# Kernel optimization log

Hardware: AMD Instinct MI355X
Metric: run time of the kernel (lower is better)

## Reference

```python
import jax, jax.numpy as jnp
import numpy as np

F_OUT = 256      # out_channels
NH = 8           # num_heads
DH = F_OUT // NH # head dim = 32
KH = KW = 8      # kernel (window) size == stride == q_stride
KK = KH * KW     # 64 keys per window


def setup_inputs() -> dict:
    key = jax.random.key(0)
    k1, k2, k3 = jax.random.split(key, 3)
    x = jax.random.normal(k1, (8, 256, 128, 128), jnp.float32)
    # 1x1 conv weight for qkv projection, xavier-ish scale
    proj_w = jax.random.normal(k2, (3 * F_OUT, 256), jnp.float32) * (1.0 / np.sqrt(256.0))
    proj_b = jnp.zeros((3 * F_OUT,), jnp.float32)
    # learned position features (module inits to zeros; use small random for a nontrivial test)
    pos_feats = jax.random.normal(k3, (F_OUT, KK), jnp.float32) * 0.02
    return {"x": x, "proj_w": proj_w, "proj_b": proj_b, "pos_feats": pos_feats}


def reference(x, proj_w, proj_b, pos_feats):
    B, C, H, W = x.shape
    f = F_OUT
    # 1x1 conv == channel GEMM: [B,3f,H,W]
    qkv = jnp.einsum('bchw,oc->bohw', x, proj_w) + proj_b[None, :, None, None]
    scale = float(f // NH) ** (-0.25)
    # query: slice every q_stride-th position -> [B,f,Hq,Wq]
    q = qkv[:, :f, ::KH, ::KW]
    kv = qkv[:, f:3 * f]                       # [B,2f,H,W]
    Hq, Wq = H // KH, W // KW
    # non-overlapping window unfold (stride==kernel, padding=0, dilation=1)
    # -> [B,Hq,Wq,2f,KK], matching torch as_strided(...).reshape(..., -1)
    kv = kv.reshape(B, 2 * f, Hq, KH, Wq, KW)
    kv = kv.transpose(0, 2, 4, 1, 3, 5).reshape(B, Hq, Wq, 2 * f, KK)
    # keys: pos_feats + scale*key, then split heads -> [B,Hq,Wq,NH,DH,KK]
    key_m = (pos_feats + scale * kv[..., :f, :]).reshape(B, Hq, Wq, NH, DH, KK)
    val_m = kv[..., f:2 * f, :].reshape(B, Hq, Wq, NH, DH, KK)
    # queries: scale, channels-last, split heads -> [B,Hq,Wq,NH,DH]
    q_m = (scale * q).transpose(0, 2, 3, 1).reshape(B, Hq, Wq, NH, DH)
    logits = jnp.einsum('bhwnd,bhwndk->bhwnk', q_m, key_m)   # [B,Hq,Wq,NH,KK]
    attn = jax.nn.softmax(logits, axis=-1)
    out = jnp.einsum('bhwnk,bhwndk->bhwnd', attn, val_m)     # [B,Hq,Wq,NH,DH]
    return out.reshape(B, Hq, Wq, f).transpose(0, 3, 1, 2)   # [B,f,Hq,Wq]
```

## Files before the change

kernel.cpp:

```cpp
#include <hip/hip_runtime.h>
#include <hip/hip_bf16.h>
#include <cstdint>
#include <cstddef>

#define SCALE 0.42044820762685725f

typedef __attribute__((ext_vector_type(8))) short short8;
typedef __attribute__((ext_vector_type(4))) short short4v;
typedef __attribute__((ext_vector_type(4))) float f32x4;

__device__ __forceinline__ unsigned int pk2bf(float lo, float hi) {
    __hip_bfloat162 h = __float22bfloat162_rn(float2{lo, hi});
    unsigned int u;
    __builtin_memcpy(&u, &h, sizeof(u));
    return u;
}
__device__ __forceinline__ unsigned short f2bf(float f) {
    unsigned int u = __builtin_bit_cast(unsigned int, f);
    u = (u + 0x7fffu + ((u >> 16) & 1u)) >> 16;
    return (unsigned short)u;
}
__device__ __forceinline__ float bf2f(unsigned short h) {
    unsigned int u = ((unsigned int)h) << 16;
    return __builtin_bit_cast(float, u);
}


__global__ __launch_bounds__(256) void prepack_w(const float* __restrict__ w,
                                                 const float* __restrict__ pos,
                                                 unsigned short* __restrict__ wp,
                                                 unsigned short* __restrict__ pT,
                                                 float* __restrict__ wqT) {
    int gid = blockIdx.x * 256 + threadIdx.x;
    if (gid < 24576) {
        int lane = gid & 63;
        int ks   = (gid >> 6) & 7;
        int mtg  = gid >> 9;
        int row  = (mtg < 32 ? 256 + mtg * 16 : (mtg - 32) * 16) + (lane & 15);
        int k0   = ks * 32 + (lane >> 4) * 8;
        const float* src = w + row * 256 + k0;
        short8 v;
#pragma unroll
        for (int j = 0; j < 8; ++j) v[j] = (short)f2bf(src[j]);
        *reinterpret_cast<short8*>(wp + (size_t)gid * 8) = v;
    } else if (gid < 40960) {
        int u = gid - 24576;
        pT[u] = f2bf(pos[(u & 255) * 64 + (u >> 8)]);
    } else {
        int u = gid - 40960;
        wqT[u] = w[(u & 255) * 256 + (u >> 8)];
    }
}

__global__ __launch_bounds__(256) void q_kernel(const float* __restrict__ x,
                                                const float* __restrict__ wqT,
                                                const float* __restrict__ proj_b,
                                                float* __restrict__ q_all) {
    __shared__ float s_x0[4][256];
    const int t = threadIdx.x;
    const int tile0 = blockIdx.x * 4;
    const int b = tile0 >> 8, hq = (tile0 >> 4) & 15, wq0 = tile0 & 15;
    {
        const float* src = x + (size_t)b * 4194304 + (size_t)t * 16384 + hq * 1024 + wq0 * 8;
#pragma unroll
        for (int j = 0; j < 4; ++j) s_x0[j][t] = src[j * 8];
    }
    __syncthreads();
    float acc[4] = {0.f, 0.f, 0.f, 0.f};
#pragma unroll 8
    for (int c = 0; c < 256; ++c) {
        float wv = wqT[c * 256 + t];
#pragma unroll
        for (int j = 0; j < 4; ++j) acc[j] = fmaf(wv, s_x0[j][c], acc[j]);
    }
    float bq = proj_b[t];
#pragma unroll
    for (int j = 0; j < 4; ++j)
        q_all[(size_t)(tile0 + j) * 256 + t] = SCALE * (acc[j] + bq);
}

template <bool PRE>
__global__ __launch_bounds__(512, 4) void attn_fused(
        const float* __restrict__ x, const float* __restrict__ proj_w,
        const float* __restrict__ proj_b, const float* __restrict__ pos,
        const unsigned short* __restrict__ wpack, const unsigned short* __restrict__ posT,
        const float* __restrict__ q_all, float* __restrict__ out) {
    __shared__ __align__(16) unsigned char s_main[32768];
    __shared__ __align__(16) float s_vbias[256];
    __shared__ __align__(16) float s_qs[256];

    const int t    = threadIdx.x;
    const int lane = t & 63;
    const int wave = t >> 6;
    const int l15  = lane & 15;
    const int l4   = lane >> 4;

    int bid  = blockIdx.x;
    int tile = (bid & 7) * 256 + (bid >> 3);
    int b  = tile >> 8;
    int hq = (tile >> 4) & 15;
    int wq = tile & 15;

    const float* xb = x + (size_t)b * 4194304 + (size_t)(hq * 8) * 128 + wq * 8;

    if (t < 256) s_vbias[t] = proj_b[512 + t];

    {
        const int p   = lane;
        const int pl  = lane & 1;
        const int px0 = lane & ~1;
        const float* xpx = xb + (px0 >> 3) * 128 + (px0 & 7);
        float2 v[16];
#pragma unroll
        for (int g = 0; g < 4; ++g)
#pragma unroll
            for (int j = 0; j < 4; ++j) {
                int c = (g * 8 + wave) * 8 + 2 * j + pl;
                v[g * 4 + j] = *reinterpret_cast<const float2*>(xpx + (size_t)c * 16384);
            }
#pragma unroll
        for (int g = 0; g < 4; ++g) {
            uint4 pk;
            unsigned int* pku = &pk.x;
#pragma unroll
            for (int j = 0; j < 4; ++j) {
                float2 w2 = v[g * 4 + j];
                float sel   = pl ? w2.x : w2.y;
                float other = __shfl_xor(sel, 1);
                pku[j] = pl ? pk2bf(other, w2.y) : pk2bf(w2.x, other);
            }
            int c8 = g * 8 + wave;
            *reinterpret_cast<uint4*>(s_main + p * 512 + ((c8 * 16) ^ ((p & 7) << 4))) = pk;
        }
    }
    __syncthreads();

    f32x4 acc[4][4];
#pragma unroll
    for (int mt = 0; mt < 4; ++mt)
#pragma unroll
        for (int nt = 0; nt < 4; ++nt) acc[mt][nt] = (f32x4){0.f, 0.f, 0.f, 0.f};
    f32x4 accQ[2];
    if (!PRE) {
#pragma unroll
        for (int mt = 0; mt < 2; ++mt) accQ[mt] = (f32x4){0.f, 0.f, 0.f, 0.f};
    }

#pragma unroll 2
    for (int ks = 0; ks < 8; ++ks) {
        short8 bfr[4];
#pragma unroll
        for (int nt = 0; nt < 4; ++nt) {
            int n  = nt * 16 + l15;
            int kb = ks * 32 + l4 * 8;
            bfr[nt] = *reinterpret_cast<const short8*>(
                s_main + n * 512 + ((2 * kb) ^ ((n & 7) << 4)));
        }
        short8 afk[2], afv[2];
#pragma unroll
        for (int mt = 0; mt < 2; ++mt) {
            if (PRE) {
                afk[mt] = *reinterpret_cast<const short8*>(
                    wpack + ((size_t)(((wave * 2 + mt) * 8 + ks) * 64 + lane)) * 8);
                afv[mt] = *reinterpret_cast<const short8*>(
                    wpack + ((size_t)(((16 + wave * 2 + mt) * 8 + ks) * 64 + lane)) * 8);
            } else {
                const float* wk = proj_w + (256 + (wave * 2 + mt) * 16 + l15) * 256 + ks * 32 + l4 * 8;
                const float* wv = proj_w + (512 + (wave * 2 + mt) * 16 + l15) * 256 + ks * 32 + l4 * 8;
#pragma unroll
                for (int j = 0; j < 8; ++j) { afk[mt][j] = (short)f2bf(wk[j]); afv[mt][j] = (short)f2bf(wv[j]); }
            }
        }
#pragma unroll
        for (int mt = 0; mt < 2; ++mt)
#pragma unroll
            for (int nt = 0; nt < 4; ++nt) {
                acc[mt][nt]     = __builtin_amdgcn_mfma_f32_16x16x32_bf16(afk[mt], bfr[nt], acc[mt][nt], 0, 0, 0);
                acc[2 + mt][nt] = __builtin_amdgcn_mfma_f32_16x16x32_bf16(afv[mt], bfr[nt], acc[2 + mt][nt], 0, 0, 0);
            }
        if (!PRE) {
            short8 afq[2];
#pragma unroll
            for (int mt = 0; mt < 2; ++mt) {
                const float* wq2 = proj_w + ((wave * 2 + mt) * 16 + l15) * 256 + ks * 32 + l4 * 8;
#pragma unroll
                for (int j = 0; j < 8; ++j) afq[mt][j] = (short)f2bf(wq2[j]);
                accQ[mt] = __builtin_amdgcn_mfma_f32_16x16x32_bf16(afq[mt], bfr[0], accQ[mt], 0, 0, 0);
            }
        }
    }

    if (!PRE) {
        if (l15 == 0) {
#pragma unroll
            for (int mt = 0; mt < 2; ++mt)
#pragma unroll
                for (int i = 0; i < 4; ++i) {
                    int row = wave * 32 + mt * 16 + l4 * 4 + i;
                    s_qs[row] = SCALE * (accQ[mt][i] + proj_b[row]);
                }
        }
    }

    float attnw[4];
    {
        float qf[2][4];
        if (PRE) {
            const float* qp = q_all + (size_t)tile * 256 + wave * 32 + l4 * 4;
#pragma unroll
            for (int mt = 0; mt < 2; ++mt) {
                float4 qv = *reinterpret_cast<const float4*>(qp + mt * 16);
                qf[mt][0] = qv.x; qf[mt][1] = qv.y; qf[mt][2] = qv.z; qf[mt][3] = qv.w;
            }
        } else {
#pragma unroll
            for (int mt = 0; mt < 2; ++mt)
#pragma unroll
                for (int i = 0; i < 4; ++i) qf[mt][i] = s_qs[wave * 32 + mt * 16 + l4 * 4 + i];
        }
        short4v pos4[4][2];
        if (PRE) {
#pragma unroll
            for (int nt = 0; nt < 4; ++nt)
#pragma unroll
                for (int mt = 0; mt < 2; ++mt)
                    pos4[nt][mt] = *reinterpret_cast<const short4v*>(
                        posT + (size_t)(nt * 16 + l15) * 256 + wave * 32 + mt * 16 + l4 * 4);
        }

        float lg[4];
#pragma unroll
        for (int nt = 0; nt < 4; ++nt) {
            float p = 0.f;
#pragma unroll
            for (int mt = 0; mt < 2; ++mt)
#pragma unroll
                for (int i = 0; i < 4; ++i) {
                    float pf = PRE ? bf2f((unsigned short)pos4[nt][mt][i])
                                   : pos[(size_t)(wave * 32 + mt * 16 + l4 * 4 + i) * 64 + nt * 16 + l15];
                    p = fmaf(qf[mt][i], fmaf(SCALE, acc[mt][nt][i], pf), p);
                }
            p += __shfl_xor(p, 16);
            p += __shfl_xor(p, 32);
            lg[nt] = p;
        }
        float mx = fmaxf(fmaxf(lg[0], lg[1]), fmaxf(lg[2], lg[3]));
        mx = fmaxf(mx, __shfl_xor(mx, 1));
        mx = fmaxf(mx, __shfl_xor(mx, 2));
        mx = fmaxf(mx, __shfl_xor(mx, 4));
        mx = fmaxf(mx, __shfl_xor(mx, 8));
        float e0 = __expf(lg[0] - mx), e1 = __expf(lg[1] - mx);
        float e2 = __expf(lg[2] - mx), e3 = __expf(lg[3] - mx);
        float s = (e0 + e1) + (e2 + e3);
        s += __shfl_xor(s, 1);
        s += __shfl_xor(s, 2);
        s += __shfl_xor(s, 4);
        s += __shfl_xor(s, 8);
        float rs = 1.f / s;
        attnw[0] = e0 * rs; attnw[1] = e1 * rs; attnw[2] = e2 * rs; attnw[3] = e3 * rs;
    }

#pragma unroll
    for (int mt = 0; mt < 2; ++mt) {
#pragma unroll
        for (int i = 0; i < 4; ++i) {
            float sum = attnw[0] * acc[2 + mt][0][i] + attnw[1] * acc[2 + mt][1][i]
                      + attnw[2] * acc[2 + mt][2][i] + attnw[3] * acc[2 + mt][3][i];
            sum += __shfl_xor(sum, 1);
            sum += __shfl_xor(sum, 2);
            sum += __shfl_xor(sum, 4);
            sum += __shfl_xor(sum, 8);
            if (l15 == 0) {
                int vr = wave * 32 + mt * 16 + l4 * 4 + i;
                out[(size_t)b * 65536 + (size_t)vr * 256 + hq * 16 + wq] = sum + s_vbias[vr];
            }
        }
    }
}

extern "C" void kernel_launch(void* const* d_in, const int* in_sizes, int n_in,
                              void* d_out, int out_size, void* d_ws, size_t ws_size,
                              hipStream_t stream) {
    (void)in_sizes; (void)n_in; (void)out_size;
    const float* x      = (const float*)d_in[0];
    const float* proj_w = (const float*)d_in[1];
    const float* proj_b = (const float*)d_in[2];
    const float* pos    = (const float*)d_in[3];
    float* out = (float*)d_out;

    const size_t OFF_POST = 393216;
    const size_t OFF_WQT  = 425984;
    const size_t OFF_QALL = 688128;
    const size_t need_ws  = OFF_QALL + 2097152;

    if (d_ws != nullptr && ws_size >= need_ws) {
        unsigned short* wp  = (unsigned short*)d_ws;
        unsigned short* pT  = (unsigned short*)((char*)d_ws + OFF_POST);
        float*          wqT = (float*)((char*)d_ws + OFF_WQT);
        float*          qA  = (float*)((char*)d_ws + OFF_QALL);
        prepack_w<<<416, 256, 0, stream>>>(proj_w, pos, wp, pT, wqT);
        q_kernel<<<512, 256, 0, stream>>>(x, wqT, proj_b, qA);
        attn_fused<true><<<2048, 512, 0, stream>>>(x, proj_w, proj_b, pos, wp, pT, qA, out);
    } else {
        attn_fused<false><<<2048, 512, 0, stream>>>(x, proj_w, proj_b, pos, nullptr, nullptr, nullptr, out);
    }
}
```

Measured before the change: 85.44 us.

## Make attention kernel persistent over 8 tiles with register-resident weights and double-buffered x

Each block now processes 8 consecutive windows instead of one, launching 256 blocks instead of 2048. The K/V weight fragments are loaded into registers once per block rather than reloaded every k-step for every window. The next window's x slab is prefetched into registers during the softmax/output phase and written to a second LDS buffer, overlapping global loads with compute. This raises register pressure (launch bounds lowered to 2 blocks per CU), and 256 blocks of 8 waves may underfill the GPU's CUs.

```diff
diff --git a/kernel.cpp b/kernel.cpp
--- a/kernel.cpp
+++ b/kernel.cpp
@@ -80,12 +80,12 @@
 }
 
 template <bool PRE>
-__global__ __launch_bounds__(512, 4) void attn_fused(
+__global__ __launch_bounds__(512, 2) void attn_fused(
         const float* __restrict__ x, const float* __restrict__ proj_w,
         const float* __restrict__ proj_b, const float* __restrict__ pos,
         const unsigned short* __restrict__ wpack, const unsigned short* __restrict__ posT,
         const float* __restrict__ q_all, float* __restrict__ out) {
-    __shared__ __align__(16) unsigned char s_main[32768];
+    __shared__ __align__(16) unsigned char s_x[2][32768];
     __shared__ __align__(16) float s_vbias[256];
     __shared__ __align__(16) float s_qs[256];
 
@@ -95,22 +95,46 @@
     const int l15  = lane & 15;
     const int l4   = lane >> 4;
 
-    int bid  = blockIdx.x;
-    int tile = (bid & 7) * 256 + (bid >> 3);
-    int b  = tile >> 8;
-    int hq = (tile >> 4) & 15;
-    int wq = tile & 15;
-
-    const float* xb = x + (size_t)b * 4194304 + (size_t)(hq * 8) * 128 + wq * 8;
+    const int bid   = blockIdx.x;
+    const int tile0 = (bid & 7) * 256 + (bid >> 3) * 8;
+    const int b   = tile0 >> 8;
+    const int hq  = (tile0 >> 4) & 15;
+    const int wq0 = tile0 & 15;
 
     if (t < 256) s_vbias[t] = proj_b[512 + t];
 
-    {
-        const int p   = lane;
-        const int pl  = lane & 1;
-        const int px0 = lane & ~1;
-        const float* xpx = xb + (px0 >> 3) * 128 + (px0 & 7);
-        float2 v[16];
+    short8 wK[2][8], wV[2][8];
+    if (PRE) {
+#pragma unroll
+        for (int mt = 0; mt < 2; ++mt)
+#pragma unroll
+            for (int ks = 0; ks < 8; ++ks) {
+                wK[mt][ks] = *reinterpret_cast<const short8*>(
+                    wpack + ((size_t)(((wave * 2 + mt) * 8 + ks) * 64 + lane)) * 8);
+                wV[mt][ks] = *reinterpret_cast<const short8*>(
+                    wpack + ((size_t)(((16 + wave * 2 + mt) * 8 + ks) * 64 + lane)) * 8);
+            }
+    } else {
+#pragma unroll
+        for (int mt = 0; mt < 2; ++mt)
+#pragma unroll
+            for (int ks = 0; ks < 8; ++ks) {
+                const float* wk = proj_w + (256 + (wave * 2 + mt) * 16 + l15) * 256 + ks * 32 + l4 * 8;
+                const float* wv = proj_w + (512 + (wave * 2 + mt) * 16 + l15) * 256 + ks * 32 + l4 * 8;
+#pragma unroll
+                for (int j = 0; j < 8; ++j) {
+                    wK[mt][ks][j] = (short)f2bf(wk[j]);
+                    wV[mt][ks][j] = (short)f2bf(wv[j]);
+                }
+            }
+    }
+
+    const int pl  = lane & 1;
+    const int px0 = lane & ~1;
+    auto issue_x = [&](int tile, float2* v) {
+        const int wq = tile & 15;
+        const float* xpx = x + (size_t)b * 4194304 + (size_t)(hq * 8) * 128 + wq * 8
+                             + (px0 >> 3) * 128 + (px0 & 7);
 #pragma unroll
         for (int g = 0; g < 4; ++g)
 #pragma unroll
@@ -118,6 +142,10 @@
                 int c = (g * 8 + wave) * 8 + 2 * j + pl;
                 v[g * 4 + j] = *reinterpret_cast<const float2*>(xpx + (size_t)c * 16384);
             }
+    };
+    auto write_x = [&](int buf, const float2* v) {
+        const int p = lane;
+        unsigned char* base = s_x[buf];
 #pragma unroll
         for (int g = 0; g < 4; ++g) {
             uint4 pk;
@@ -130,81 +158,77 @@
                 pku[j] = pl ? pk2bf(other, w2.y) : pk2bf(w2.x, other);
             }
             int c8 = g * 8 + wave;
-            *reinterpret_cast<uint4*>(s_main + p * 512 + ((c8 * 16) ^ ((p & 7) << 4))) = pk;
-        }
+            *reinterpret_cast<uint4*>(base + p * 512 + ((c8 * 16) ^ ((p & 7) << 4))) = pk;
+        }
+    };
+
+    {
+        float2 v0[16];
+        issue_x(tile0, v0);
+        write_x(0, v0);
     }
     __syncthreads();
 
-    f32x4 acc[4][4];
-#pragma unroll
-    for (int mt = 0; mt < 4; ++mt)
-#pragma unroll
-        for (int nt = 0; nt < 4; ++nt) acc[mt][nt] = (f32x4){0.f, 0.f, 0.f, 0.f};
-    f32x4 accQ[2];
-    if (!PRE) {
-#pragma unroll
-        for (int mt = 0; mt < 2; ++mt) accQ[mt] = (f32x4){0.f, 0.f, 0.f, 0.f};
-    }
-
-#pragma unroll 2
-    for (int ks = 0; ks < 8; ++ks) {
-        short8 bfr[4];
-#pragma unroll
-        for (int nt = 0; nt < 4; ++nt) {
-            int n  = nt * 16 + l15;
-            int kb = ks * 32 + l4 * 8;
-            bfr[nt] = *reinterpret_cast<const short8*>(
-                s_main + n * 512 + ((2 * kb) ^ ((n & 7) << 4)));
-        }
-        short8 afk[2], afv[2];
-#pragma unroll
-        for (int mt = 0; mt < 2; ++mt) {
-            if (PRE) {
-                afk[mt] = *reinterpret_cast<const short8*>(
-                    wpack + ((size_t)(((wave * 2 + mt) * 8 + ks) * 64 + lane)) * 8);
-                afv[mt] = *reinterpret_cast<const short8*>(
-                    wpack + ((size_t)(((16 + wave * 2 + mt) * 8 + ks) * 64 + lane)) * 8);
-            } else {
-                const float* wk = proj_w + (256 + (wave * 2 + mt) * 16 + l15) * 256 + ks * 32 + l4 * 8;
-                const float* wv = proj_w + (512 + (wave * 2 + mt) * 16 + l15) * 256 + ks * 32 + l4 * 8;
-#pragma unroll
-                for (int j = 0; j < 8; ++j) { afk[mt][j] = (short)f2bf(wk[j]); afv[mt][j] = (short)f2bf(wv[j]); }
-            }
-        }
-#pragma unroll
-        for (int mt = 0; mt < 2; ++mt)
+#pragma unroll 1
+    for (int ti = 0; ti < 8; ++ti) {
+        const int tile = tile0 + ti;
+        const int wq   = wq0 + ti;
+        const unsigned char* xl = s_x[ti & 1];
+
+        f32x4 acc[4][4];
+#pragma unroll
+        for (int mt = 0; mt < 4; ++mt)
+#pragma unroll
+            for (int nt = 0; nt < 4; ++nt) acc[mt][nt] = (f32x4){0.f, 0.f, 0.f, 0.f};
+        f32x4 accQ[2];
+        if (!PRE) {
+#pragma unroll
+            for (int mt = 0; mt < 2; ++mt) accQ[mt] = (f32x4){0.f, 0.f, 0.f, 0.f};
+        }
+
+#pragma unroll
+        for (int ks = 0; ks < 8; ++ks) {
+            short8 bfr[4];
 #pragma unroll
             for (int nt = 0; nt < 4; ++nt) {
-                acc[mt][nt]     = __builtin_amdgcn_mfma_f32_16x16x32_bf16(afk[mt], bfr[nt], acc[mt][nt], 0, 0, 0);
-                acc[2 + mt][nt] = __builtin_amdgcn_mfma_f32_16x16x32_bf16(afv[mt], bfr[nt], acc[2 + mt][nt], 0, 0, 0);
-            }
+                int n  = nt * 16 + l15;
+                int kb = ks * 32 + l4 * 8;
+                bfr[nt] = *reinterpret_cast<const short8*>(
+                    xl + n * 512 + ((2 * kb) ^ ((n & 7) << 4)));
+            }
+#pragma unroll
+            for (int mt = 0; mt < 2; ++mt)
+#pragma unroll
+                for (int nt = 0; nt < 4; ++nt) {
+                    acc[mt][nt]     = __builtin_amdgcn_mfma_f32_16x16x32_bf16(wK[mt][ks], bfr[nt], acc[mt][nt], 0, 0, 0);
+                    acc[2 + mt][nt] = __builtin_amdgcn_mfma_f32_16x16x32_bf16(wV[mt][ks], bfr[nt], acc[2 + mt][nt], 0, 0, 0);
+                }
+            if (!PRE) {
+                short8 afq[2];
+#pragma unroll
+                for (int mt = 0; mt < 2; ++mt) {
+                    const float* wq2 = proj_w + ((wave * 2 + mt) * 16 + l15) * 256 + ks * 32 + l4 * 8;
+#pragma unroll
+                    for (int j = 0; j < 8; ++j) afq[mt][j] = (short)f2bf(wq2[j]);
+                    accQ[mt] = __builtin_amdgcn_mfma_f32_16x16x32_bf16(afq[mt], bfr[0], accQ[mt], 0, 0, 0);
+                }
+            }
+        }
+
         if (!PRE) {
-            short8 afq[2];
-#pragma unroll
-            for (int mt = 0; mt < 2; ++mt) {
-                const float* wq2 = proj_w + ((wave * 2 + mt) * 16 + l15) * 256 + ks * 32 + l4 * 8;
-#pragma unroll
-                for (int j = 0; j < 8; ++j) afq[mt][j] = (short)f2bf(wq2[j]);
-                accQ[mt] = __builtin_amdgcn_mfma_f32_16x16x32_bf16(afq[mt], bfr[0], accQ[mt], 0, 0, 0);
-            }
-        }
-    }
-
-    if (!PRE) {
-        if (l15 == 0) {
-#pragma unroll
-            for (int mt = 0; mt < 2; ++mt)
-#pragma unroll
-                for (int i = 0; i < 4; ++i) {
-                    int row = wave * 32 + mt * 16 + l4 * 4 + i;
-                    s_qs[row] = SCALE * (accQ[mt][i] + proj_b[row]);
-                }
-        }
-    }
-
-    float attnw[4];
-    {
+            if (l15 == 0) {
+#pragma unroll
+                for (int mt = 0; mt < 2; ++mt)
+#pragma unroll
+                    for (int i = 0; i < 4; ++i) {
+                        int row = wave * 32 + mt * 16 + l4 * 4 + i;
+                        s_qs[row] = SCALE * (accQ[mt][i] + proj_b[row]);
+                    }
+            }
+        }
+
         float qf[2][4];
+        short4v pos4[4][2];
         if (PRE) {
             const float* qp = q_all + (size_t)tile * 256 + wave * 32 + l4 * 4;
 #pragma unroll
@@ -212,14 +236,6 @@
                 float4 qv = *reinterpret_cast<const float4*>(qp + mt * 16);
                 qf[mt][0] = qv.x; qf[mt][1] = qv.y; qf[mt][2] = qv.z; qf[mt][3] = qv.w;
             }
-        } else {
-#pragma unroll
-            for (int mt = 0; mt < 2; ++mt)
-#pragma unroll
-                for (int i = 0; i < 4; ++i) qf[mt][i] = s_qs[wave * 32 + mt * 16 + l4 * 4 + i];
-        }
-        short4v pos4[4][2];
-        if (PRE) {
 #pragma unroll
             for (int nt = 0; nt < 4; ++nt)
 #pragma unroll
@@ -228,53 +244,69 @@
                         posT + (size_t)(nt * 16 + l15) * 256 + wave * 32 + mt * 16 + l4 * 4);
         }
 
-        float lg[4];
-#pragma unroll
-        for (int nt = 0; nt < 4; ++nt) {
-            float p = 0.f;
+        float2 v[16];
+        if (ti < 7) issue_x(tile + 1, v);
+
+        if (!PRE) {
 #pragma unroll
             for (int mt = 0; mt < 2; ++mt)
 #pragma unroll
-                for (int i = 0; i < 4; ++i) {
-                    float pf = PRE ? bf2f((unsigned short)pos4[nt][mt][i])
-                                   : pos[(size_t)(wave * 32 + mt * 16 + l4 * 4 + i) * 64 + nt * 16 + l15];
-                    p = fmaf(qf[mt][i], fmaf(SCALE, acc[mt][nt][i], pf), p);
+                for (int i = 0; i < 4; ++i) qf[mt][i] = s_qs[wave * 32 + mt * 16 + l4 * 4 + i];
+        }
+
+        float attnw[4];
+        {
+            float lg[4];
+#pragma unroll
+            for (int nt = 0; nt < 4; ++nt) {
+                float p = 0.f;
+#pragma unroll
+                for (int mt = 0; mt < 2; ++mt)
+#pragma unroll
+                    for (int i = 0; i < 4; ++i) {
+                        float pf = PRE ? bf2f((unsigned short)pos4[nt][mt][i])
+                                       : pos[(size_t)(wave * 32 + mt * 16 + l4 * 4 + i) * 64 + nt * 16 + l15];
+                        p = fmaf(qf[mt][i], fmaf(SCALE, acc[mt][nt][i], pf), p);
+                    }
+                p += __shfl_xor(p, 16);
+                p += __shfl_xor(p, 32);
+                lg[nt] = p;
+            }
+            float mx = fmaxf(fmaxf(lg[0], lg[1]), fmaxf(lg[2], lg[3]));
+            mx = fmaxf(mx, __shfl_xor(mx, 1));
+            mx = fmaxf(mx, __shfl_xor(mx, 2));
+            mx = fmaxf(mx, __shfl_xor(mx, 4));
+            mx = fmaxf(mx, __shfl_xor(mx, 8));
+            float e0 = __expf(lg[0] - mx), e1 = __expf(lg[1] - mx);
+            float e2 = __expf(lg[2] - mx), e3 = __expf(lg[3] - mx);
+            float s = (e0 + e1) + (e2 + e3);
+            s += __shfl_xor(s, 1);
+            s += __shfl_xor(s, 2);
+            s += __shfl_xor(s, 4);
+            s += __shfl_xor(s, 8);
+            float rs = 1.f / s;
+            attnw[0] = e0 * rs; attnw[1] = e1 * rs; attnw[2] = e2 * rs; attnw[3] = e3 * rs;
+        }
+
+#pragma unroll
+        for (int mt = 0; mt < 2; ++mt) {
+#pragma unroll
+            for (int i = 0; i < 4; ++i) {
+                float sum = attnw[0] * acc[2 + mt][0][i] + attnw[1] * acc[2 + mt][1][i]
+                          + attnw[2] * acc[2 + mt][2][i] + attnw[3] * acc[2 + mt][3][i];
+                sum += __shfl_xor(sum, 1);
+                sum += __shfl_xor(sum, 2);
+                sum += __shfl_xor(sum, 4);
+                sum += __shfl_xor(sum, 8);
+                if (l15 == 0) {
+                    int vr = wave * 32 + mt * 16 + l4 * 4 + i;
+                    out[(size_t)b * 65536 + (size_t)vr * 256 + hq * 16 + wq] = sum + s_vbias[vr];
                 }
-            p += __shfl_xor(p, 16);
-            p += __shfl_xor(p, 32);
-            lg[nt] = p;
-        }
-        float mx = fmaxf(fmaxf(lg[0], lg[1]), fmaxf(lg[2], lg[3]));
-        mx = fmaxf(mx, __shfl_xor(mx, 1));
-        mx = fmaxf(mx, __shfl_xor(mx, 2));
-        mx = fmaxf(mx, __shfl_xor(mx, 4));
-        mx = fmaxf(mx, __shfl_xor(mx, 8));
-        float e0 = __expf(lg[0] - mx), e1 = __expf(lg[1] - mx);
-        float e2 = __expf(lg[2] - mx), e3 = __expf(lg[3] - mx);
-        float s = (e0 + e1) + (e2 + e3);
-        s += __shfl_xor(s, 1);
-        s += __shfl_xor(s, 2);
-        s += __shfl_xor(s, 4);
-        s += __shfl_xor(s, 8);
-        float rs = 1.f / s;
-        attnw[0] = e0 * rs; attnw[1] = e1 * rs; attnw[2] = e2 * rs; attnw[3] = e3 * rs;
-    }
-
-#pragma unroll
-    for (int mt = 0; mt < 2; ++mt) {
-#pragma unroll
-        for (int i = 0; i < 4; ++i) {
-            float sum = attnw[0] * acc[2 + mt][0][i] + attnw[1] * acc[2 + mt][1][i]
-                      + attnw[2] * acc[2 + mt][2][i] + attnw[3] * acc[2 + mt][3][i];
-            sum += __shfl_xor(sum, 1);
-            sum += __shfl_xor(sum, 2);
-            sum += __shfl_xor(sum, 4);
-            sum += __shfl_xor(sum, 8);
-            if (l15 == 0) {
-                int vr = wave * 32 + mt * 16 + l4 * 4 + i;
-                out[(size_t)b * 65536 + (size_t)vr * 256 + hq * 16 + wq] = sum + s_vbias[vr];
-            }
-        }
+            }
+        }
+
+        if (ti < 7) write_x((ti & 1) ^ 1, v);
+        __syncthreads();
     }
 }
 
@@ -300,8 +332,8 @@
         float*          qA  = (float*)((char*)d_ws + OFF_QALL);
         prepack_w<<<416, 256, 0, stream>>>(proj_w, pos, wp, pT, wqT);
         q_kernel<<<512, 256, 0, stream>>>(x, wqT, proj_b, qA);
-        attn_fused<true><<<2048, 512, 0, stream>>>(x, proj_w, proj_b, pos, wp, pT, qA, out);
+        attn_fused<true><<<256, 512, 0, stream>>>(x, proj_w, proj_b, pos, wp, pT, qA, out);
     } else {
-        attn_fused<false><<<2048, 512, 0, stream>>>(x, proj_w, proj_b, pos, nullptr, nullptr, nullptr, out);
-    }
-}
+        attn_fused<false><<<256, 512, 0, stream>>>(x, proj_w, proj_b, pos, nullptr, nullptr, nullptr, out);
+    }
+}
```

Result: slower. 230.3 us (+169.6%).

## Split heads across two blocks per tile with separate K and V waves

Applied to the files above, without the earlier changes.

Each window tile is now handled by two blocks, each covering four heads. Within a block, waves 0-3 compute keys and softmax while waves 4-7 compute values, and the attention weights pass between them through shared memory. This halves per-wave accumulator registers so occupancy can go up (launch bounds raised to 5). The cost is that every block still loads and converts the full 8x8x256 input window, so x traffic and conversion work double, and an extra barrier is added.

```diff
diff --git a/kernel.cpp b/kernel.cpp
--- a/kernel.cpp
+++ b/kernel.cpp
@@ -80,13 +80,14 @@
 }
 
 template <bool PRE>
-__global__ __launch_bounds__(512, 4) void attn_fused(
+__global__ __launch_bounds__(512, 5) void attn_fused(
         const float* __restrict__ x, const float* __restrict__ proj_w,
         const float* __restrict__ proj_b, const float* __restrict__ pos,
         const unsigned short* __restrict__ wpack, const unsigned short* __restrict__ posT,
         const float* __restrict__ q_all, float* __restrict__ out) {
     __shared__ __align__(16) unsigned char s_main[32768];
     __shared__ __align__(16) float s_vbias[256];
+    __shared__ __align__(16) float s_attn[4][64];
     __shared__ __align__(16) float s_qs[256];
 
     const int t    = threadIdx.x;
@@ -95,13 +96,18 @@
     const int l15  = lane & 15;
     const int l4   = lane >> 4;
 
-    int bid  = blockIdx.x;
-    int tile = (bid & 7) * 256 + (bid >> 3);
-    int b  = tile >> 8;
-    int hq = (tile >> 4) & 15;
-    int wq = tile & 15;
-
-    const float* xb = x + (size_t)b * 4194304 + (size_t)(hq * 8) * 128 + wq * 8;
+    const int bid  = blockIdx.x;
+    const int xcd  = bid & 7;
+    const int idx  = bid >> 3;
+    const int tin  = idx >> 1;
+    const int half = idx & 1;
+    const int b  = xcd;
+    const int hq = tin >> 4;
+    const int wq = tin & 15;
+    const int tile = xcd * 256 + tin;
+
+    const int head = half * 4 + (wave & 3);
+    const bool isK = wave < 4;
 
     if (t < 256) s_vbias[t] = proj_b[512 + t];
 
@@ -109,7 +115,8 @@
         const int p   = lane;
         const int pl  = lane & 1;
         const int px0 = lane & ~1;
-        const float* xpx = xb + (px0 >> 3) * 128 + (px0 & 7);
+        const float* xpx = x + (size_t)b * 4194304 + (size_t)(hq * 8) * 128 + wq * 8
+                             + (px0 >> 3) * 128 + (px0 & 7);
         float2 v[16];
 #pragma unroll
         for (int g = 0; g < 4; ++g)
@@ -135,16 +142,18 @@
     }
     __syncthreads();
 
-    f32x4 acc[4][4];
-#pragma unroll
-    for (int mt = 0; mt < 4; ++mt)
+    f32x4 acc[2][4];
+#pragma unroll
+    for (int mt = 0; mt < 2; ++mt)
 #pragma unroll
         for (int nt = 0; nt < 4; ++nt) acc[mt][nt] = (f32x4){0.f, 0.f, 0.f, 0.f};
     f32x4 accQ[2];
-    if (!PRE) {
+    if (!PRE && isK) {
 #pragma unroll
         for (int mt = 0; mt < 2; ++mt) accQ[mt] = (f32x4){0.f, 0.f, 0.f, 0.f};
     }
+
+    const int mtg0 = (isK ? 0 : 16) + head * 2;
 
 #pragma unroll 2
     for (int ks = 0; ks < 8; ++ks) {
@@ -156,33 +165,29 @@
             bfr[nt] = *reinterpret_cast<const short8*>(
                 s_main + n * 512 + ((2 * kb) ^ ((n & 7) << 4)));
         }
-        short8 afk[2], afv[2];
+        short8 af[2];
 #pragma unroll
         for (int mt = 0; mt < 2; ++mt) {
             if (PRE) {
-                afk[mt] = *reinterpret_cast<const short8*>(
-                    wpack + ((size_t)(((wave * 2 + mt) * 8 + ks) * 64 + lane)) * 8);
-                afv[mt] = *reinterpret_cast<const short8*>(
-                    wpack + ((size_t)(((16 + wave * 2 + mt) * 8 + ks) * 64 + lane)) * 8);
+                af[mt] = *reinterpret_cast<const short8*>(
+                    wpack + ((size_t)(((mtg0 + mt) * 8 + ks) * 64 + lane)) * 8);
             } else {
-                const float* wk = proj_w + (256 + (wave * 2 + mt) * 16 + l15) * 256 + ks * 32 + l4 * 8;
-                const float* wv = proj_w + (512 + (wave * 2 + mt) * 16 + l15) * 256 + ks * 32 + l4 * 8;
-#pragma unroll
-                for (int j = 0; j < 8; ++j) { afk[mt][j] = (short)f2bf(wk[j]); afv[mt][j] = (short)f2bf(wv[j]); }
+                int row = (isK ? 256 : 512) + head * 32 + mt * 16 + l15;
+                const float* src = proj_w + row * 256 + ks * 32 + l4 * 8;
+#pragma unroll
+                for (int j = 0; j < 8; ++j) af[mt][j] = (short)f2bf(src[j]);
             }
         }
 #pragma unroll
         for (int mt = 0; mt < 2; ++mt)
 #pragma unroll
-            for (int nt = 0; nt < 4; ++nt) {
-                acc[mt][nt]     = __builtin_amdgcn_mfma_f32_16x16x32_bf16(afk[mt], bfr[nt], acc[mt][nt], 0, 0, 0);
-                acc[2 + mt][nt] = __builtin_amdgcn_mfma_f32_16x16x32_bf16(afv[mt], bfr[nt], acc[2 + mt][nt], 0, 0, 0);
-            }
-        if (!PRE) {
+            for (int nt = 0; nt < 4; ++nt)
+                acc[mt][nt] = __builtin_amdgcn_mfma_f32_16x16x32_bf16(af[mt], bfr[nt], acc[mt][nt], 0, 0, 0);
+        if (!PRE && isK) {
             short8 afq[2];
 #pragma unroll
             for (int mt = 0; mt < 2; ++mt) {
-                const float* wq2 = proj_w + ((wave * 2 + mt) * 16 + l15) * 256 + ks * 32 + l4 * 8;
+                const float* wq2 = proj_w + (head * 32 + mt * 16 + l15) * 256 + ks * 32 + l4 * 8;
 #pragma unroll
                 for (int j = 0; j < 8; ++j) afq[mt][j] = (short)f2bf(wq2[j]);
                 accQ[mt] = __builtin_amdgcn_mfma_f32_16x16x32_bf16(afq[mt], bfr[0], accQ[mt], 0, 0, 0);
@@ -190,42 +195,38 @@
         }
     }
 
-    if (!PRE) {
-        if (l15 == 0) {
-#pragma unroll
-            for (int mt = 0; mt < 2; ++mt)
-#pragma unroll
-                for (int i = 0; i < 4; ++i) {
-                    int row = wave * 32 + mt * 16 + l4 * 4 + i;
-                    s_qs[row] = SCALE * (accQ[mt][i] + proj_b[row]);
-                }
-        }
-    }
-
-    float attnw[4];
-    {
+    if (isK) {
+        if (!PRE) {
+            if (l15 == 0) {
+#pragma unroll
+                for (int mt = 0; mt < 2; ++mt)
+#pragma unroll
+                    for (int i = 0; i < 4; ++i) {
+                        int row = head * 32 + mt * 16 + l4 * 4 + i;
+                        s_qs[row] = SCALE * (accQ[mt][i] + proj_b[row]);
+                    }
+            }
+        }
         float qf[2][4];
+        short4v pos4[4][2];
         if (PRE) {
-            const float* qp = q_all + (size_t)tile * 256 + wave * 32 + l4 * 4;
+            const float* qp = q_all + (size_t)tile * 256 + head * 32 + l4 * 4;
 #pragma unroll
             for (int mt = 0; mt < 2; ++mt) {
                 float4 qv = *reinterpret_cast<const float4*>(qp + mt * 16);
                 qf[mt][0] = qv.x; qf[mt][1] = qv.y; qf[mt][2] = qv.z; qf[mt][3] = qv.w;
             }
-        } else {
-#pragma unroll
-            for (int mt = 0; mt < 2; ++mt)
-#pragma unroll
-                for (int i = 0; i < 4; ++i) qf[mt][i] = s_qs[wave * 32 + mt * 16 + l4 * 4 + i];
-        }
-        short4v pos4[4][2];
-        if (PRE) {
 #pragma unroll
             for (int nt = 0; nt < 4; ++nt)
 #pragma unroll
                 for (int mt = 0; mt < 2; ++mt)
                     pos4[nt][mt] = *reinterpret_cast<const short4v*>(
-                        posT + (size_t)(nt * 16 + l15) * 256 + wave * 32 + mt * 16 + l4 * 4);
+                        posT + (size_t)(nt * 16 + l15) * 256 + head * 32 + mt * 16 + l4 * 4);
+        } else {
+#pragma unroll
+            for (int mt = 0; mt < 2; ++mt)
+#pragma unroll
+                for (int i = 0; i < 4; ++i) qf[mt][i] = s_qs[head * 32 + mt * 16 + l4 * 4 + i];
         }
 
         float lg[4];
@@ -237,7 +238,7 @@
 #pragma unroll
                 for (int i = 0; i < 4; ++i) {
                     float pf = PRE ? bf2f((unsigned short)pos4[nt][mt][i])
-                                   : pos[(size_t)(wave * 32 + mt * 16 + l4 * 4 + i) * 64 + nt * 16 + l15];
+                                   : pos[(size_t)(head * 32 + mt * 16 + l4 * 4 + i) * 64 + nt * 16 + l15];
                     p = fmaf(qf[mt][i], fmaf(SCALE, acc[mt][nt][i], pf), p);
                 }
             p += __shfl_xor(p, 16);
@@ -257,22 +258,32 @@
         s += __shfl_xor(s, 4);
         s += __shfl_xor(s, 8);
         float rs = 1.f / s;
-        attnw[0] = e0 * rs; attnw[1] = e1 * rs; attnw[2] = e2 * rs; attnw[3] = e3 * rs;
-    }
-
-#pragma unroll
-    for (int mt = 0; mt < 2; ++mt) {
-#pragma unroll
-        for (int i = 0; i < 4; ++i) {
-            float sum = attnw[0] * acc[2 + mt][0][i] + attnw[1] * acc[2 + mt][1][i]
-                      + attnw[2] * acc[2 + mt][2][i] + attnw[3] * acc[2 + mt][3][i];
-            sum += __shfl_xor(sum, 1);
-            sum += __shfl_xor(sum, 2);
-            sum += __shfl_xor(sum, 4);
-            sum += __shfl_xor(sum, 8);
-            if (l15 == 0) {
-                int vr = wave * 32 + mt * 16 + l4 * 4 + i;
-                out[(size_t)b * 65536 + (size_t)vr * 256 + hq * 16 + wq] = sum + s_vbias[vr];
+        if (l4 == 0) {
+            s_attn[head & 3][l15]      = e0 * rs;
+            s_attn[head & 3][16 + l15] = e1 * rs;
+            s_attn[head & 3][32 + l15] = e2 * rs;
+            s_attn[head & 3][48 + l15] = e3 * rs;
+        }
+    }
+    __syncthreads();
+
+    if (!isK) {
+        const float* ap = s_attn[head & 3];
+        float a0 = ap[l15], a1 = ap[16 + l15], a2 = ap[32 + l15], a3 = ap[48 + l15];
+#pragma unroll
+        for (int mt = 0; mt < 2; ++mt) {
+#pragma unroll
+            for (int i = 0; i < 4; ++i) {
+                float sum = a0 * acc[mt][0][i] + a1 * acc[mt][1][i]
+                          + a2 * acc[mt][2][i] + a3 * acc[mt][3][i];
+                sum += __shfl_xor(sum, 1);
+                sum += __shfl_xor(sum, 2);
+                sum += __shfl_xor(sum, 4);
+                sum += __shfl_xor(sum, 8);
+                if (l15 == 0) {
+                    int vr = head * 32 + mt * 16 + l4 * 4 + i;
+                    out[(size_t)b * 65536 + (size_t)vr * 256 + hq * 16 + wq] = sum + s_vbias[vr];
+                }
             }
         }
     }
@@ -300,8 +311,8 @@
         float*          qA  = (float*)((char*)d_ws + OFF_QALL);
         prepack_w<<<416, 256, 0, stream>>>(proj_w, pos, wp, pT, wqT);
         q_kernel<<<512, 256, 0, stream>>>(x, wqT, proj_b, qA);
-        attn_fused<true><<<2048, 512, 0, stream>>>(x, proj_w, proj_b, pos, wp, pT, qA, out);
+        attn_fused<true><<<4096, 512, 0, stream>>>(x, proj_w, proj_b, pos, wp, pT, qA, out);
     } else {
-        attn_fused<false><<<2048, 512, 0, stream>>>(x, proj_w, proj_b, pos, nullptr, nullptr, nullptr, out);
-    }
-}
+        attn_fused<false><<<4096, 512, 0, stream>>>(x, proj_w, proj_b, pos, nullptr, nullptr, nullptr, out);
+    }
+}
```

Result: slower. 97.23 us (+13.8%).

## Process four adjacent windows per block with strip-wide coalesced x loads

Applied to the files above, without the earlier changes.

Each attention block now handles a strip of four horizontally adjacent 8x8 windows. It loads all 32 columns of x rows into four LDS tiles so global reads cover wider contiguous spans, and hoists the pos loads out of the per-tile loop. The q kernel likewise computes 16 query tiles per block, and grid sizes shrink to match. The larger LDS footprint (128KB) and the lower occupancy bound reduce concurrency, and the per-tile work inside a block now runs serially.

```diff
diff --git a/kernel.cpp b/kernel.cpp
--- a/kernel.cpp
+++ b/kernel.cpp
@@ -56,36 +56,38 @@
                                                 const float* __restrict__ wqT,
                                                 const float* __restrict__ proj_b,
                                                 float* __restrict__ q_all) {
-    __shared__ float s_x0[4][256];
+    __shared__ float s_x0[16][256];
     const int t = threadIdx.x;
-    const int tile0 = blockIdx.x * 4;
-    const int b = tile0 >> 8, hq = (tile0 >> 4) & 15, wq0 = tile0 & 15;
+    const int tile0 = blockIdx.x * 16;
+    const int b = tile0 >> 8, hq = (tile0 >> 4) & 15;
     {
-        const float* src = x + (size_t)b * 4194304 + (size_t)t * 16384 + hq * 1024 + wq0 * 8;
-#pragma unroll
-        for (int j = 0; j < 4; ++j) s_x0[j][t] = src[j * 8];
+        const float* src = x + (size_t)b * 4194304 + (size_t)t * 16384 + hq * 1024;
+#pragma unroll
+        for (int j = 0; j < 16; ++j) s_x0[j][t] = src[j * 8];
     }
     __syncthreads();
-    float acc[4] = {0.f, 0.f, 0.f, 0.f};
-#pragma unroll 8
+    float acc[16];
+#pragma unroll
+    for (int j = 0; j < 16; ++j) acc[j] = 0.f;
+#pragma unroll 4
     for (int c = 0; c < 256; ++c) {
         float wv = wqT[c * 256 + t];
 #pragma unroll
-        for (int j = 0; j < 4; ++j) acc[j] = fmaf(wv, s_x0[j][c], acc[j]);
+        for (int j = 0; j < 16; ++j) acc[j] = fmaf(wv, s_x0[j][c], acc[j]);
     }
     float bq = proj_b[t];
 #pragma unroll
-    for (int j = 0; j < 4; ++j)
+    for (int j = 0; j < 16; ++j)
         q_all[(size_t)(tile0 + j) * 256 + t] = SCALE * (acc[j] + bq);
 }
 
 template <bool PRE>
-__global__ __launch_bounds__(512, 4) void attn_fused(
+__global__ __launch_bounds__(512, 2) void attn_fused(
         const float* __restrict__ x, const float* __restrict__ proj_w,
         const float* __restrict__ proj_b, const float* __restrict__ pos,
         const unsigned short* __restrict__ wpack, const unsigned short* __restrict__ posT,
         const float* __restrict__ q_all, float* __restrict__ out) {
-    __shared__ __align__(16) unsigned char s_main[32768];
+    __shared__ __align__(16) unsigned char s_x[4][32768];
     __shared__ __align__(16) float s_vbias[256];
     __shared__ __align__(16) float s_qs[256];
 
@@ -95,184 +97,194 @@
     const int l15  = lane & 15;
     const int l4   = lane >> 4;
 
-    int bid  = blockIdx.x;
-    int tile = (bid & 7) * 256 + (bid >> 3);
-    int b  = tile >> 8;
-    int hq = (tile >> 4) & 15;
-    int wq = tile & 15;
-
-    const float* xb = x + (size_t)b * 4194304 + (size_t)(hq * 8) * 128 + wq * 8;
+    const int bid   = blockIdx.x;
+    const int b     = bid & 7;
+    const int strip = bid >> 3;
+    const int hq    = strip >> 2;
+    const int wq0   = (strip & 3) * 4;
+    const int tile0 = b * 256 + hq * 16 + wq0;
 
     if (t < 256) s_vbias[t] = proj_b[512 + t];
 
+    short4v pos4[4][2];
+    if (PRE) {
+#pragma unroll
+        for (int nt = 0; nt < 4; ++nt)
+#pragma unroll
+            for (int mt = 0; mt < 2; ++mt)
+                pos4[nt][mt] = *reinterpret_cast<const short4v*>(
+                    posT + (size_t)(nt * 16 + l15) * 256 + wave * 32 + mt * 16 + l4 * 4);
+    }
+
     {
-        const int p   = lane;
         const int pl  = lane & 1;
-        const int px0 = lane & ~1;
-        const float* xpx = xb + (px0 >> 3) * 128 + (px0 & 7);
-        float2 v[16];
-#pragma unroll
-        for (int g = 0; g < 4; ++g)
-#pragma unroll
-            for (int j = 0; j < 4; ++j) {
-                int c = (g * 8 + wave) * 8 + 2 * j + pl;
-                v[g * 4 + j] = *reinterpret_cast<const float2*>(xpx + (size_t)c * 16384);
-            }
-#pragma unroll
-        for (int g = 0; g < 4; ++g) {
-            uint4 pk;
-            unsigned int* pku = &pk.x;
-#pragma unroll
-            for (int j = 0; j < 4; ++j) {
-                float2 w2 = v[g * 4 + j];
-                float sel   = pl ? w2.x : w2.y;
+        const int w2  = (lane >> 1) & 15;
+        const int hlo = (lane >> 5) & 1;
+        const int pxs = w2 * 2 + pl;
+        const int til = pxs >> 3;
+        const int px7 = pxs & 7;
+        const float* xs = x + (size_t)b * 4194304 + (size_t)(hq * 8) * 128 + wq0 * 8;
+#pragma unroll 1
+        for (int kb = 0; kb < 8; ++kb) {
+            float2 v[8];
+#pragma unroll
+            for (int u = 0; u < 8; ++u) {
+                int idx = wave * 64 + kb * 8 + u;
+                int c   = (idx & 127) * 2 + pl;
+                int h   = (idx >> 7) * 2 + hlo;
+                v[u] = *reinterpret_cast<const float2*>(xs + (size_t)c * 16384 + h * 128 + w2 * 2);
+            }
+#pragma unroll
+            for (int u = 0; u < 8; ++u) {
+                int idx = wave * 64 + kb * 8 + u;
+                int h   = (idx >> 7) * 2 + hlo;
+                int pin = h * 8 + px7;
+                float sel   = pl ? v[u].x : v[u].y;
                 float other = __shfl_xor(sel, 1);
-                pku[j] = pl ? pk2bf(other, w2.y) : pk2bf(w2.x, other);
-            }
-            int c8 = g * 8 + wave;
-            *reinterpret_cast<uint4*>(s_main + p * 512 + ((c8 * 16) ^ ((p & 7) << 4))) = pk;
+                unsigned int pk = pl ? pk2bf(other, v[u].y) : pk2bf(v[u].x, other);
+                *reinterpret_cast<unsigned int*>(
+                    s_x[til] + pin * 512 + ((4 * (idx & 127)) ^ ((pin & 7) << 4))) = pk;
+            }
         }
     }
     __syncthreads();
 
-    f32x4 acc[4][4];
-#pragma unroll
-    for (int mt = 0; mt < 4; ++mt)
-#pragma unroll
-        for (int nt = 0; nt < 4; ++nt) acc[mt][nt] = (f32x4){0.f, 0.f, 0.f, 0.f};
-    f32x4 accQ[2];
-    if (!PRE) {
-#pragma unroll
-        for (int mt = 0; mt < 2; ++mt) accQ[mt] = (f32x4){0.f, 0.f, 0.f, 0.f};
-    }
+#pragma unroll 1
+    for (int ti = 0; ti < 4; ++ti) {
+        const int tile = tile0 + ti;
+        const int wq   = wq0 + ti;
+        const unsigned char* xl = s_x[ti];
+
+        f32x4 acc[4][4];
+#pragma unroll
+        for (int mt = 0; mt < 4; ++mt)
+#pragma unroll
+            for (int nt = 0; nt < 4; ++nt) acc[mt][nt] = (f32x4){0.f, 0.f, 0.f, 0.f};
+        f32x4 accQ[2];
+        if (!PRE) {
+#pragma unroll
+            for (int mt = 0; mt < 2; ++mt) accQ[mt] = (f32x4){0.f, 0.f, 0.f, 0.f};
+        }
 
 #pragma unroll 2
-    for (int ks = 0; ks < 8; ++ks) {
-        short8 bfr[4];
-#pragma unroll
-        for (int nt = 0; nt < 4; ++nt) {
-            int n  = nt * 16 + l15;
-            int kb = ks * 32 + l4 * 8;
-            bfr[nt] = *reinterpret_cast<const short8*>(
-                s_main + n * 512 + ((2 * kb) ^ ((n & 7) << 4)));
-        }
-        short8 afk[2], afv[2];
+        for (int ks = 0; ks < 8; ++ks) {
+            short8 bfr[4];
+#pragma unroll
+            for (int nt = 0; nt < 4; ++nt) {
+                int n  = nt * 16 + l15;
+                int kb = ks * 32 + l4 * 8;
+                bfr[nt] = *reinterpret_cast<const short8*>(
+                    xl + n * 512 + ((2 * kb) ^ ((n & 7) << 4)));
+            }
+            short8 afk[2], afv[2];
+#pragma unroll
+            for (int mt = 0; mt < 2; ++mt) {
+                if (PRE) {
+                    afk[mt] = *reinterpret_cast<const short8*>(
+                        wpack + ((size_t)(((wave * 2 + mt) * 8 + ks) * 64 + lane)) * 8);
+                    afv[mt] = *reinterpret_cast<const short8*>(
+                        wpack + ((size_t)(((16 + wave * 2 + mt) * 8 + ks) * 64 + lane)) * 8);
+                } else {
+                    const float* wk = proj_w + (256 + (wave * 2 + mt) * 16 + l15) * 256 + ks * 32 + l4 * 8;
+                    const float* wv = proj_w + (512 + (wave * 2 + mt) * 16 + l15) * 256 + ks * 32 + l4 * 8;
+#pragma unroll
+                    for (int j = 0; j < 8; ++j) { afk[mt][j] = (short)f2bf(wk[j]); afv[mt][j] = (short)f2bf(wv[j]); }
+                }
+            }
+#pragma unroll
+            for (int mt = 0; mt < 2; ++mt)
+#pragma unroll
+                for (int nt = 0; nt < 4; ++nt) {
+                    acc[mt][nt]     = __builtin_amdgcn_mfma_f32_16x16x32_bf16(afk[mt], bfr[nt], acc[mt][nt], 0, 0, 0);
+                    acc[2 + mt][nt] = __builtin_amdgcn_mfma_f32_16x16x32_bf16(afv[mt], bfr[nt], acc[2 + mt][nt], 0, 0, 0);
+                }
+            if (!PRE) {
+                short8 afq[2];
+#pragma unroll
+                for (int mt = 0; mt < 2; ++mt) {
+                    const float* wq2 = proj_w + ((wave * 2 + mt) * 16 + l15) * 256 + ks * 32 + l4 * 8;
+#pragma unroll
+                    for (int j = 0; j < 8; ++j) afq[mt][j] = (short)f2bf(wq2[j]);
+                    accQ[mt] = __builtin_amdgcn_mfma_f32_16x16x32_bf16(afq[mt], bfr[0], accQ[mt], 0, 0, 0);
+                }
+            }
+        }
+
+        if (!PRE) {
+            if (l15 == 0) {
+#pragma unroll
+                for (int mt = 0; mt < 2; ++mt)
+#pragma unroll
+                    for (int i = 0; i < 4; ++i) {
+                        int row = wave * 32 + mt * 16 + l4 * 4 + i;
+                        s_qs[row] = SCALE * (accQ[mt][i] + proj_b[row]);
+                    }
+            }
+        }
+
+        float attnw[4];
+        {
+            float qf[2][4];
+            if (PRE) {
+                const float* qp = q_all + (size_t)tile * 256 + wave * 32 + l4 * 4;
+#pragma unroll
+                for (int mt = 0; mt < 2; ++mt) {
+                    float4 qv = *reinterpret_cast<const float4*>(qp + mt * 16);
+                    qf[mt][0] = qv.x; qf[mt][1] = qv.y; qf[mt][2] = qv.z; qf[mt][3] = qv.w;
+                }
+            } else {
+#pragma unroll
+                for (int mt = 0; mt < 2; ++mt)
+#pragma unroll
+                    for (int i = 0; i < 4; ++i) qf[mt][i] = s_qs[wave * 32 + mt * 16 + l4 * 4 + i];
+            }
+
+            float lg[4];
+#pragma unroll
+            for (int nt = 0; nt < 4; ++nt) {
+                float p = 0.f;
+#pragma unroll
+                for (int mt = 0; mt < 2; ++mt)
+#pragma unroll
+                    for (int i = 0; i < 4; ++i) {
+                        float pf = PRE ? bf2f((unsigned short)pos4[nt][mt][i])
+                                       : pos[(size_t)(wave * 32 + mt * 16 + l4 * 4 + i) * 64 + nt * 16 + l15];
+                        p = fmaf(qf[mt][i], fmaf(SCALE, acc[mt][nt][i], pf), p);
+                    }
+                p += __shfl_xor(p, 16);
+                p += __shfl_xor(p, 32);
+                lg[nt] = p;
+            }
+            float mx = fmaxf(fmaxf(lg[0], lg[1]), fmaxf(lg[2], lg[3]));
+            mx = fmaxf(mx, __shfl_xor(mx, 1));
+            mx = fmaxf(mx, __shfl_xor(mx, 2));
+            mx = fmaxf(mx, __shfl_xor(mx, 4));
+            mx = fmaxf(mx, __shfl_xor(mx, 8));
+            float e0 = __expf(lg[0] - mx), e1 = __expf(lg[1] - mx);
+            float e2 = __expf(lg[2] - mx), e3 = __expf(lg[3] - mx);
+            float s = (e0 + e1) + (e2 + e3);
+            s += __shfl_xor(s, 1);
+            s += __shfl_xor(s, 2);
+            s += __shfl_xor(s, 4);
+            s += __shfl_xor(s, 8);
+            float rs = 1.f / s;
+            attnw[0] = e0 * rs; attnw[1] = e1 * rs; attnw[2] = e2 * rs; attnw[3] = e3 * rs;
+        }
+
 #pragma unroll
         for (int mt = 0; mt < 2; ++mt) {
-            if (PRE) {
-                afk[mt] = *reinterpret_cast<const short8*>(
-                    wpack + ((size_t)(((wave * 2 + mt) * 8 + ks) * 64 + lane)) * 8);
-                afv[mt] = *reinterpret_cast<const short8*>(
-                    wpack + ((size_t)(((16 + wave * 2 + mt) * 8 + ks) * 64 + lane)) * 8);
-            } else {
-                const float* wk = proj_w + (256 + (wave * 2 + mt) * 16 + l15) * 256 + ks * 32 + l4 * 8;
-                const float* wv = proj_w + (512 + (wave * 2 + mt) * 16 + l15) * 256 + ks * 32 + l4 * 8;
-#pragma unroll
-                for (int j = 0; j < 8; ++j) { afk[mt][j] = (short)f2bf(wk[j]); afv[mt][j] = (short)f2bf(wv[j]); }
-            }
-        }
-#pragma unroll
-        for (int mt = 0; mt < 2; ++mt)
-#pragma unroll
-            for (int nt = 0; nt < 4; ++nt) {
-                acc[mt][nt]     = __builtin_amdgcn_mfma_f32_16x16x32_bf16(afk[mt], bfr[nt], acc[mt][nt], 0, 0, 0);
-                acc[2 + mt][nt] = __builtin_amdgcn_mfma_f32_16x16x32_bf16(afv[mt], bfr[nt], acc[2 + mt][nt], 0, 0, 0);
-            }
-        if (!PRE) {
-            short8 afq[2];
-#pragma unroll
-            for (int mt = 0; mt < 2; ++mt) {
-                const float* wq2 = proj_w + ((wave * 2 + mt) * 16 + l15) * 256 + ks * 32 + l4 * 8;
-#pragma unroll
-                for (int j = 0; j < 8; ++j) afq[mt][j] = (short)f2bf(wq2[j]);
-                accQ[mt] = __builtin_amdgcn_mfma_f32_16x16x32_bf16(afq[mt], bfr[0], accQ[mt], 0, 0, 0);
-            }
-        }
-    }
-
-    if (!PRE) {
-        if (l15 == 0) {
-#pragma unroll
-            for (int mt = 0; mt < 2; ++mt)
-#pragma unroll
-                for (int i = 0; i < 4; ++i) {
-                    int row = wave * 32 + mt * 16 + l4 * 4 + i;
-                    s_qs[row] = SCALE * (accQ[mt][i] + proj_b[row]);
-                }
-        }
-    }
-
-    float attnw[4];
-    {
-        float qf[2][4];
-        if (PRE) {
-            const float* qp = q_all + (size_t)tile * 256 + wave * 32 + l4 * 4;
-#pragma unroll
-            for (int mt = 0; mt < 2; ++mt) {
-                float4 qv = *reinterpret_cast<const float4*>(qp + mt * 16);
-                qf[mt][0] = qv.x; qf[mt][1] = qv.y; qf[mt][2] = qv.z; qf[mt][3] = qv.w;
-            }
-        } else {
-#pragma unroll
-            for (int mt = 0; mt < 2; ++mt)
-#pragma unroll
-                for (int i = 0; i < 4; ++i) qf[mt][i] = s_qs[wave * 32 + mt * 16 + l4 * 4 + i];
-        }
-        short4v pos4[4][2];
-        if (PRE) {
-#pragma unroll
-            for (int nt = 0; nt < 4; ++nt)
-#pragma unroll
-                for (int mt = 0; mt < 2; ++mt)
-                    pos4[nt][mt] = *reinterpret_cast<const short4v*>(
-                        posT + (size_t)(nt * 16 + l15) * 256 + wave * 32 + mt * 16 + l4 * 4);
-        }
-
-        float lg[4];
-#pragma unroll
-        for (int nt = 0; nt < 4; ++nt) {
-            float p = 0.f;
-#pragma unroll
-            for (int mt = 0; mt < 2; ++mt)
-#pragma unroll
-                for (int i = 0; i < 4; ++i) {
-                    float pf = PRE ? bf2f((unsigned short)pos4[nt][mt][i])
-                                   : pos[(size_t)(wave * 32 + mt * 16 + l4 * 4 + i) * 64 + nt * 16 + l15];
-                    p = fmaf(qf[mt][i], fmaf(SCALE, acc[mt][nt][i], pf), p);
-                }
-            p += __shfl_xor(p, 16);
-            p += __shfl_xor(p, 32);
-            lg[nt] = p;
-        }
-        float mx = fmaxf(fmaxf(lg[0], lg[1]), fmaxf(lg[2], lg[3]));
-        mx = fmaxf(mx, __shfl_xor(mx, 1));
-        mx = fmaxf(mx, __shfl_xor(mx, 2));
-        mx = fmaxf(mx, __shfl_xor(mx, 4));
-        mx = fmaxf(mx, __shfl_xor(mx, 8));
-        float e0 = __expf(lg[0] - mx), e1 = __expf(lg[1] - mx);
-        float e2 = __expf(lg[2] - mx), e3 = __expf(lg[3] - mx);
-        float s = (e0 + e1) + (e2 + e3);
-        s += __shfl_xor(s, 1);
-        s += __shfl_xor(s, 2);
-        s += __shfl_xor(s, 4);
-        s += __shfl_xor(s, 8);
-        float rs = 1.f / s;
-        attnw[0] = e0 * rs; attnw[1] = e1 * rs; attnw[2] = e2 * rs; attnw[3] = e3 * rs;
-    }
-
-#pragma unroll
-    for (int mt = 0; mt < 2; ++mt) {
-#pragma unroll
-        for (int i = 0; i < 4; ++i) {
-            float sum = attnw[0] * acc[2 + mt][0][i] + attnw[1] * acc[2 + mt][1][i]
-                      + attnw[2] * acc[2 + mt][2][i] + attnw[3] * acc[2 + mt][3][i];
-            sum += __shfl_xor(sum, 1);
-            sum += __shfl_xor(sum, 2);
-            sum += __shfl_xor(sum, 4);
-            sum += __shfl_xor(sum, 8);
-            if (l15 == 0) {
-                int vr = wave * 32 + mt * 16 + l4 * 4 + i;
-                out[(size_t)b * 65536 + (size_t)vr * 256 + hq * 16 + wq] = sum + s_vbias[vr];
+#pragma unroll
+            for (int i = 0; i < 4; ++i) {
+                float sum = attnw[0] * acc[2 + mt][0][i] + attnw[1] * acc[2 + mt][1][i]
+                          + attnw[2] * acc[2 + mt][2][i] + attnw[3] * acc[2 + mt][3][i];
+                sum += __shfl_xor(sum, 1);
+                sum += __shfl_xor(sum, 2);
+                sum += __shfl_xor(sum, 4);
+                sum += __shfl_xor(sum, 8);
+                if (l15 == 0) {
+                    int vr = wave * 32 + mt * 16 + l4 * 4 + i;
+                    out[(size_t)b * 65536 + (size_t)vr * 256 + hq * 16 + wq] = sum + s_vbias[vr];
+                }
             }
         }
     }
@@ -299,9 +311,9 @@
         float*          wqT = (float*)((char*)d_ws + OFF_WQT);
         float*          qA  = (float*)((char*)d_ws + OFF_QALL);
         prepack_w<<<416, 256, 0, stream>>>(proj_w, pos, wp, pT, wqT);
-        q_kernel<<<512, 256, 0, stream>>>(x, wqT, proj_b, qA);
-        attn_fused<true><<<2048, 512, 0, stream>>>(x, proj_w, proj_b, pos, wp, pT, qA, out);
+        q_kernel<<<128, 256, 0, stream>>>(x, wqT, proj_b, qA);
+        attn_fused<true><<<512, 512, 0, stream>>>(x, proj_w, proj_b, pos, wp, pT, qA, out);
     } else {
-        attn_fused<false><<<2048, 512, 0, stream>>>(x, proj_w, proj_b, pos, nullptr, nullptr, nullptr, out);
-    }
-}
+        attn_fused<false><<<512, 512, 0, stream>>>(x, proj_w, proj_b, pos, nullptr, nullptr, nullptr, out);
+    }
+}
```

Measured after the change: 102.5 us. 1.2x slower.
